# Optimization experiments

Hardware: AMD Instinct MI355X
Metric: run time of the kernel (lower is better)

Reference implementation:

```python
import jax, jax.numpy as jnp
import numpy as np

NEG_SLOPE = 0.2  # PyG GATConv default


def gat_layer(x, src, dst, W, a_src, a_dst, b, heads, ch, num_nodes):
    # x: [N, F_in]; W: [F_in, heads*ch]; a_src/a_dst: [heads, ch]; b: [heads*ch]
    h = (x @ W).reshape(num_nodes, heads, ch)                      # [N,H,C]
    al_s = jnp.einsum('nhc,hc->nh', h, a_src)                      # [N,H]
    al_d = jnp.einsum('nhc,hc->nh', h, a_dst)                      # [N,H]
    e = jax.nn.leaky_relu(al_s[src] + al_d[dst], NEG_SLOPE)        # [E,H]
    # segment softmax over incoming edges of each destination node
    emax = jax.ops.segment_max(e, dst, num_segments=num_nodes)     # [N,H]
    ee = jnp.exp(e - emax[dst])
    denom = jax.ops.segment_sum(ee, dst, num_segments=num_nodes)   # [N,H]
    alpha = ee / denom[dst]                                        # [E,H]
    msg = h[src] * alpha[..., None]                                # [E,H,C]
    out = jax.ops.segment_sum(msg, dst, num_segments=num_nodes)    # [N,H,C]
    return out.reshape(num_nodes, heads * ch) + b


def setup_inputs() -> dict:
    key = jax.random.key(0)
    ks = jax.random.split(key, 12)
    N, F_in, H1, C1, OUT = 50000, 128, 6, 32, 2
    E = 800000
    x = jax.random.normal(ks[0], (N, F_in), dtype=jnp.float32)
    edge_index = jax.random.randint(ks[1], (2, E), 0, N, dtype=jnp.int64)
    s = 0.1
    return {
        'x': x,
        'edge_index': edge_index,
        'W1': jax.random.normal(ks[2], (F_in, H1 * C1), dtype=jnp.float32) * s,
        'a1_src': jax.random.normal(ks[3], (H1, C1), dtype=jnp.float32) * s,
        'a1_dst': jax.random.normal(ks[4], (H1, C1), dtype=jnp.float32) * s,
        'b1': jnp.zeros((H1 * C1,), dtype=jnp.float32),
        'W2': jax.random.normal(ks[5], (H1 * C1, 1 * OUT), dtype=jnp.float32) * s,
        'a2_src': jax.random.normal(ks[6], (1, OUT), dtype=jnp.float32) * s,
        'a2_dst': jax.random.normal(ks[7], (1, OUT), dtype=jnp.float32) * s,
        'b2': jnp.zeros((OUT,), dtype=jnp.float32),
    }


def reference(x, edge_index, W1, a1_src, a1_dst, b1, W2, a2_src, a2_dst, b2):
    N = x.shape[0]
    loop = jnp.arange(N, dtype=edge_index.dtype)
    src = jnp.concatenate([edge_index[0], loop])  # add_self_loops=True (PyG default)
    dst = jnp.concatenate([edge_index[1], loop])
    h = gat_layer(x, src, dst, W1, a1_src, a1_dst, b1, heads=6, ch=32, num_nodes=N)
    h = jax.nn.relu(h)
    h = gat_layer(h, src, dst, W2, a2_src, a2_dst, b2, heads=1, ch=2, num_nodes=N)
    return jax.nn.log_softmax(h, axis=1)
```

## Files before the change

kernel.cpp:

```cpp
#include <hip/hip_runtime.h>
#include <hip/hip_fp16.h>

#define LRELU(v) ((v) > 0.0f ? (v) : 0.2f * (v))

constexpr int F_IN = 128;
constexpr int NH1  = 6;
constexpr int D1   = 192;

typedef _Float16 half8 __attribute__((ext_vector_type(8)));
typedef float floatx4 __attribute__((ext_vector_type(4)));

__device__ __forceinline__ void wave_lds_fence() {
  __builtin_amdgcn_wave_barrier();
  asm volatile("s_waitcnt lgkmcnt(0)" ::: "memory");
  __builtin_amdgcn_wave_barrier();
}

__global__ __launch_bounds__(256) void k_hist(const float* __restrict__ W1,
                                              __half* __restrict__ w1t,
                                              const int* __restrict__ dst,
                                              int* __restrict__ cnt,
                                              int* __restrict__ pose, int N, int E) {
  int tid = blockIdx.x * 256 + threadIdx.x;
  if (tid < F_IN * D1) {
    int k = tid / D1, n = tid - k * D1;
    w1t[(size_t)n * F_IN + k] = __float2half(W1[tid]);
  }
  if (tid < E) {
    int s = blockIdx.x & 7;
    pose[tid] = atomicAdd(&cnt[s * N + dst[tid]], 1);
  }
}

__global__ __launch_bounds__(256) void k_gemm1(const float* __restrict__ x,
                                               const __half* __restrict__ w1t,
                                               const float* __restrict__ a1s,
                                               const float* __restrict__ a1d,
                                               __half* __restrict__ h1h,
                                               float* __restrict__ als,
                                               float* __restrict__ ald, int N) {
  int wv = blockIdx.x * 4 + (threadIdx.x >> 6);
  int m0 = wv * 16;
  if (m0 >= N) return;
  int lane = threadIdx.x & 63;
  int ln15 = lane & 15, q = lane >> 4;

  float avs[12], avd[12];
#pragma unroll
  for (int f = 0; f < 12; ++f) {
    int idx = (f >> 1) * 32 + (f & 1) * 16 + ln15;
    avs[f] = a1s[idx];
    avd[f] = a1d[idx];
  }

  floatx4 acc[12];
#pragma unroll
  for (int f = 0; f < 12; ++f) acc[f] = (floatx4){0.f, 0.f, 0.f, 0.f};

  int arowi = m0 + ln15;
  if (arowi >= N) arowi = N - 1;
  const float* arow = x + (size_t)arowi * F_IN + q * 8;
#pragma unroll
  for (int kc = 0; kc < F_IN; kc += 32) {
    float4 u0 = *(const float4*)(arow + kc);
    float4 u1 = *(const float4*)(arow + kc + 4);
    half8 a;
    a[0] = (_Float16)u0.x; a[1] = (_Float16)u0.y; a[2] = (_Float16)u0.z; a[3] = (_Float16)u0.w;
    a[4] = (_Float16)u1.x; a[5] = (_Float16)u1.y; a[6] = (_Float16)u1.z; a[7] = (_Float16)u1.w;
#pragma unroll
    for (int f = 0; f < 12; ++f) {
      half8 b = *(const half8*)(w1t + (size_t)(16 * f + ln15) * F_IN + kc + q * 8);
      acc[f] = __builtin_amdgcn_mfma_f32_16x16x32_f16(a, b, acc[f], 0, 0, 0);
    }
  }

#pragma unroll
  for (int f = 0; f < 12; ++f) {
#pragma unroll
    for (int r = 0; r < 4; ++r) {
      int n = m0 + q * 4 + r;
      if (n < N) h1h[(size_t)n * D1 + 16 * f + ln15] = __float2half(acc[f][r]);
    }
  }

#pragma unroll
  for (int r = 0; r < 4; ++r) {
    float ps[6] = {0.f, 0.f, 0.f, 0.f, 0.f, 0.f};
    float pd[6] = {0.f, 0.f, 0.f, 0.f, 0.f, 0.f};
#pragma unroll
    for (int f = 0; f < 12; ++f) {
      ps[f >> 1] = fmaf(acc[f][r], avs[f], ps[f >> 1]);
      pd[f >> 1] = fmaf(acc[f][r], avd[f], pd[f >> 1]);
    }
#pragma unroll
    for (int h = 0; h < 6; ++h) {
#pragma unroll
      for (int m = 8; m; m >>= 1) {
        ps[h] += __shfl_xor(ps[h], m);
        pd[h] += __shfl_xor(pd[h], m);
      }
    }
    float os = 0.f, od = 0.f;
#pragma unroll
    for (int h = 0; h < 6; ++h)
      if (ln15 == h) { os = ps[h]; od = pd[h]; }
    int n = m0 + q * 4 + r;
    if (ln15 < 6 && n < N) {
      als[(size_t)n * 6 + ln15] = os;
      ald[(size_t)n * 6 + ln15] = od;
    }
  }
}

__global__ void k_scanA(const int* __restrict__ cnt, int* __restrict__ spre,
                        int* __restrict__ offs, int* __restrict__ bsum, int N) {
  int t = threadIdx.x;
  int idx = blockIdx.x * 256 + t;
  int lane = t & 63, w = t >> 6;
  int run = 0;
#pragma unroll
  for (int s = 0; s < 8; ++s) {
    int c = (idx < N) ? cnt[s * N + idx] : 0;
    if (idx < N) spre[s * N + idx] = run;
    run += c;
  }
  int v = run;
  int incl = v;
#pragma unroll
  for (int d = 1; d < 64; d <<= 1) {
    int u = __shfl_up(incl, d);
    if (lane >= d) incl += u;
  }
  __shared__ int wt[4];
  if (lane == 63) wt[w] = incl;
  __syncthreads();
  int woff = 0;
  for (int i = 0; i < w; ++i) woff += wt[i];
  if (idx < N) offs[idx] = woff + incl - v;
  if (t == 255) bsum[blockIdx.x] = woff + incl;
}

__global__ void k_scanB(int* __restrict__ bsum, int* __restrict__ boff, int NB) {
  int t = threadIdx.x;
  int lane = t & 63, w = t >> 6;
  int v = (t < NB) ? bsum[t] : 0;
  int incl = v;
#pragma unroll
  for (int d = 1; d < 64; d <<= 1) {
    int u = __shfl_up(incl, d);
    if (lane >= d) incl += u;
  }
  __shared__ int wt[4];
  if (lane == 63) wt[w] = incl;
  __syncthreads();
  int woff = 0;
  for (int i = 0; i < w; ++i) woff += wt[i];
  if (t < NB) boff[t] = woff + incl - v;
}

__global__ void k_scanC(int* __restrict__ offs, const int* __restrict__ boff,
                        const int* __restrict__ bsum, int N, int NB) {
  int idx = blockIdx.x * 256 + threadIdx.x;
  if (idx < N) offs[idx] += boff[blockIdx.x];
  if (idx == 0) offs[N] = boff[NB - 1] + bsum[NB - 1];
}

__global__ __launch_bounds__(256) void k_place(const int* __restrict__ src,
                                               const int* __restrict__ dst,
                                               const int* __restrict__ offs,
                                               const int* __restrict__ spre,
                                               const int* __restrict__ pose,
                                               int* __restrict__ ssort, int N, int E) {
  int e = blockIdx.x * 256 + threadIdx.x;
  if (e < E) {
    int d = dst[e];
    int s = (e >> 8) & 7;
    ssort[offs[d] + spre[s * N + d] + pose[e]] = src[e];
  }
}

__global__ __launch_bounds__(256) void k_agg1(
    const __half* __restrict__ h1h, const float* __restrict__ als, const float* __restrict__ ald,
    const int* __restrict__ offs, const int* __restrict__ srcs,
    const float* __restrict__ b1, const float* __restrict__ W2,
    const float* __restrict__ a2s, const float* __restrict__ a2d,
    float4* __restrict__ pk, int N) {
  __shared__ float wbuf[4][64][9];
  int wid = threadIdx.x >> 6, lane = threadIdx.x & 63;
  int d = blockIdx.x * 4 + wid;
  if (d >= N) return;
  int off = offs[d], cnt = offs[d + 1] - off;
  int tot = cnt + 1;

  float aldh[6];
  {
    const float* ap = ald + (size_t)d * 6;
    float2 q0 = *(const float2*)ap, q1 = *(const float2*)(ap + 2), q2 = *(const float2*)(ap + 4);
    aldh[0] = q0.x; aldh[1] = q0.y; aldh[2] = q1.x;
    aldh[3] = q1.y; aldh[4] = q2.x; aldh[5] = q2.y;
  }

  float dh[6] = {0.f, 0.f, 0.f, 0.f, 0.f, 0.f};
  int nchunk = (tot + 63) >> 6;

  float a0 = 0.f, a1 = 0.f, a2 = 0.f;
  const int hw = lane >> 4;
  const int hh = 4 + (lane >> 5);

  auto body = [&](int j) {
    float w_a = wbuf[wid][j][hw];
    float w_b = wbuf[wid][j][hh];
    int soff = __float_as_int(wbuf[wid][j][6]);
    const __half* hp = (const __half*)((const char*)h1h + soff);
    float2 v = __half22float2(*(const __half2*)(hp + 2 * lane));
    float vh = __half2float(hp[128 + lane]);
    a0 = fmaf(w_a, v.x, a0);
    a1 = fmaf(w_a, v.y, a1);
    a2 = fmaf(w_b, vh, a2);
  };
  auto jloop = [&](int jmax) {
    int j = 0;
    for (; j + 3 < jmax; j += 4) { body(j); body(j + 1); body(j + 2); body(j + 3); }
    for (; j < jmax; ++j) body(j);
  };

  if (nchunk == 1) {
    float wreg[6];
    int sreg = 0;
    if (lane < tot) {
      int s = (lane == cnt) ? d : srcs[off + lane];
      sreg = s;
      const float* ap = als + (size_t)s * 6;
      float2 p0 = *(const float2*)ap, p1 = *(const float2*)(ap + 2), p2 = *(const float2*)(ap + 4);
      float ev[6] = {p0.x, p0.y, p1.x, p1.y, p2.x, p2.y};
#pragma unroll
      for (int h = 0; h < 6; ++h) {
        float e = ev[h] + aldh[h];
        e = LRELU(e);
        wreg[h] = __expf(e);
        dh[h] = wreg[h];
      }
    }
#pragma unroll
    for (int h = 0; h < 6; ++h) {
#pragma unroll
      for (int m = 32; m; m >>= 1) dh[h] += __shfl_xor(dh[h], m);
      dh[h] = 1.0f / dh[h];
    }
    if (lane < tot) {
#pragma unroll
      for (int h = 0; h < 6; ++h) wbuf[wid][lane][h] = wreg[h] * dh[h];
      wbuf[wid][lane][6] = __int_as_float(sreg * (D1 * 2));
    }
    wave_lds_fence();
    jloop(tot);
  } else {
    for (int c = 0; c < nchunk; ++c) {
      int i = c * 64 + lane;
      if (i < tot) {
        int s = (i == cnt) ? d : srcs[off + i];
        const float* ap = als + (size_t)s * 6;
        float2 p0 = *(const float2*)ap, p1 = *(const float2*)(ap + 2), p2 = *(const float2*)(ap + 4);
        float ev[6] = {p0.x, p0.y, p1.x, p1.y, p2.x, p2.y};
#pragma unroll
        for (int h = 0; h < 6; ++h) {
          float e = ev[h] + aldh[h];
          e = LRELU(e);
          dh[h] += __expf(e);
        }
      }
    }
#pragma unroll
    for (int h = 0; h < 6; ++h) {
#pragma unroll
      for (int m = 32; m; m >>= 1) dh[h] += __shfl_xor(dh[h], m);
      dh[h] = 1.0f / dh[h];
    }
    for (int c = 0; c < nchunk; ++c) {
      int i = c * 64 + lane;
      if (i < tot) {
        int s = (i == cnt) ? d : srcs[off + i];
        const float* ap = als + (size_t)s * 6;
        float2 p0 = *(const float2*)ap, p1 = *(const float2*)(ap + 2), p2 = *(const float2*)(ap + 4);
        float ev[6] = {p0.x, p0.y, p1.x, p1.y, p2.x, p2.y};
#pragma unroll
        for (int h = 0; h < 6; ++h) {
          float e = ev[h] + aldh[h];
          e = LRELU(e);
          wbuf[wid][lane][h] = __expf(e) * dh[h];
        }
        wbuf[wid][lane][6] = __int_as_float(s * (D1 * 2));
      }
      wave_lds_fence();
      int jmax = tot - c * 64;
      if (jmax > 64) jmax = 64;
      jloop(jmax);
      wave_lds_fence();
    }
  }

  float2 bv = *(const float2*)(b1 + 2 * lane);
  float v0 = fmaxf(a0 + bv.x, 0.f);
  float v1 = fmaxf(a1 + bv.y, 0.f);
  float v2 = fmaxf(a2 + b1[128 + lane], 0.f);
  float4 ww = *(const float4*)(W2 + 4 * lane);
  float2 wh = *(const float2*)(W2 + (128 + lane) * 2);
  float s0 = v0 * ww.x + v1 * ww.z + v2 * wh.x;
  float s1 = v0 * ww.y + v1 * ww.w + v2 * wh.y;
#pragma unroll
  for (int m = 32; m; m >>= 1) {
    s0 += __shfl_xor(s0, m);
    s1 += __shfl_xor(s1, m);
  }
  if (lane == 0) {
    pk[d] = make_float4(s0, s1,
                        s0 * a2s[0] + s1 * a2s[1],
                        s0 * a2d[0] + s1 * a2d[1]);
  }
}

__global__ __launch_bounds__(256) void k_agg2(
    const float4* __restrict__ pk, const int* __restrict__ offs,
    const int* __restrict__ srcs, const float* __restrict__ b2,
    float* __restrict__ out, int N) {
  int tid = blockIdx.x * 256 + threadIdx.x;
  int g = tid >> 3, r = tid & 7;
  if (g >= N) return;
  int off = offs[g], cnt = offs[g + 1] - off;
  int tot = cnt + 1;
  float ad = pk[g].w;
  float den = 0.f, o0 = 0.f, o1 = 0.f;
  for (int i = r; i < tot; i += 8) {
    int s = (i == cnt) ? g : srcs[off + i];
    float4 p = pk[s];
    float e = p.z + ad;
    e = LRELU(e);
    float a = __expf(e);
    den += a;
    o0 = fmaf(a, p.x, o0);
    o1 = fmaf(a, p.y, o1);
  }
#pragma unroll
  for (int m = 4; m; m >>= 1) {
    den += __shfl_xor(den, m);
    o0 += __shfl_xor(o0, m);
    o1 += __shfl_xor(o1, m);
  }
  if (r == 0) {
    float inv = 1.0f / den;
    o0 = o0 * inv + b2[0];
    o1 = o1 * inv + b2[1];
    float mm = fmaxf(o0, o1);
    float l = mm + logf(__expf(o0 - mm) + __expf(o1 - mm));
    *(float2*)(out + (size_t)g * 2) = make_float2(o0 - l, o1 - l);
  }
}

extern "C" void kernel_launch(void* const* d_in, const int* in_sizes, int n_in,
                              void* d_out, int out_size, void* d_ws, size_t ws_size,
                              hipStream_t stream) {
  const float* x   = (const float*)d_in[0];
  const int*   ei  = (const int*)d_in[1];
  const float* W1  = (const float*)d_in[2];
  const float* a1s = (const float*)d_in[3];
  const float* a1d = (const float*)d_in[4];
  const float* b1  = (const float*)d_in[5];
  const float* W2  = (const float*)d_in[6];
  const float* a2s = (const float*)d_in[7];
  const float* a2d = (const float*)d_in[8];
  const float* b2  = (const float*)d_in[9];
  float* out = (float*)d_out;

  const int N = in_sizes[0] / F_IN;
  const int E = in_sizes[1] / 2;
  const int* srcp = ei;
  const int* dstp = ei + E;

  char* w = (char*)d_ws;
  auto alloc = [&](size_t bytes) {
    char* p = w;
    w += (bytes + 255) & ~(size_t)255;
    return p;
  };
  __half* h1h   = (__half*)alloc((size_t)N * D1 * 2);
  __half* w1t   = (__half*)alloc((size_t)F_IN * D1 * 2);
  float* als    = (float*)alloc((size_t)N * NH1 * 4);
  float* ald    = (float*)alloc((size_t)N * NH1 * 4);
  float4* pk    = (float4*)alloc((size_t)N * 16);
  int*   cnt    = (int*)alloc((size_t)N * 8 * 4);
  int*   spre   = (int*)alloc((size_t)N * 8 * 4);
  int*   offs   = (int*)alloc((size_t)(N + 1) * 4);
  int*   pose   = (int*)alloc((size_t)E * 4);
  int*   bsum   = (int*)alloc(1024);
  int*   boff   = (int*)alloc(1024);
  int*   ssort  = (int*)alloc((size_t)E * 4);

  const int NB = (N + 255) / 256;

  hipMemsetAsync(cnt, 0, (size_t)N * 8 * 4, stream);

  k_hist<<<(E + 255) / 256, 256, 0, stream>>>(W1, w1t, dstp, cnt, pose, N, E);

  int nwave = (N + 15) / 16;
  k_gemm1<<<(nwave + 3) / 4, 256, 0, stream>>>(x, w1t, a1s, a1d, h1h, als, ald, N);

  k_scanA<<<NB, 256, 0, stream>>>(cnt, spre, offs, bsum, N);
  k_scanB<<<1, 256, 0, stream>>>(bsum, boff, NB);
  k_scanC<<<NB, 256, 0, stream>>>(offs, boff, bsum, N, NB);
  k_place<<<(E + 255) / 256, 256, 0, stream>>>(srcp, dstp, offs, spre, pose, ssort, N, E);

  k_agg1<<<(N + 3) / 4, 256, 0, stream>>>(h1h, als, ald, offs, ssort, b1, W2,
                                          a2s, a2d, pk, N);
  k_agg2<<<(N * 8 + 255) / 256, 256, 0, stream>>>(pk, offs, ssort, b2, out, N);
}
```

Baseline: 237.7 us.

## Fuse histogram with GEMM, stage W1 in LDS, single-block scan

Result: slower. 291.2 us (+22.5%).

```diff
diff --git a/kernel.cpp b/kernel.cpp
--- a/kernel.cpp
+++ b/kernel.cpp
@@ -16,32 +16,21 @@
   __builtin_amdgcn_wave_barrier();
 }
 
-__global__ __launch_bounds__(256) void k_hist(const float* __restrict__ W1,
-                                              __half* __restrict__ w1t,
-                                              const int* __restrict__ dst,
-                                              int* __restrict__ cnt,
-                                              int* __restrict__ pose, int N, int E) {
-  int tid = blockIdx.x * 256 + threadIdx.x;
-  if (tid < F_IN * D1) {
-    int k = tid / D1, n = tid - k * D1;
-    w1t[(size_t)n * F_IN + k] = __float2half(W1[tid]);
-  }
-  if (tid < E) {
-    int s = blockIdx.x & 7;
-    pose[tid] = atomicAdd(&cnt[s * N + dst[tid]], 1);
-  }
-}
-
-__global__ __launch_bounds__(256) void k_gemm1(const float* __restrict__ x,
-                                               const __half* __restrict__ w1t,
-                                               const float* __restrict__ a1s,
-                                               const float* __restrict__ a1d,
-                                               __half* __restrict__ h1h,
-                                               float* __restrict__ als,
-                                               float* __restrict__ ald, int N) {
-  int wv = blockIdx.x * 4 + (threadIdx.x >> 6);
+__global__ __launch_bounds__(256) void k_fused(
+    const int* __restrict__ dst, int* __restrict__ cnt, int* __restrict__ pose,
+    const float* __restrict__ x, const float* __restrict__ W1,
+    const float* __restrict__ a1s, const float* __restrict__ a1d,
+    __half* __restrict__ h1h, float* __restrict__ als, float* __restrict__ ald,
+    int N, int E, int HB) {
+  if ((int)blockIdx.x < HB) {
+    int e = blockIdx.x * 256 + threadIdx.x;
+    if (e < E) pose[e] = atomicAdd(&cnt[dst[e]], 1);
+    return;
+  }
+
+  __shared__ _Float16 wlds[192][40];
+  int wv = ((int)blockIdx.x - HB) * 4 + (threadIdx.x >> 6);
   int m0 = wv * 16;
-  if (m0 >= N) return;
   int lane = threadIdx.x & 63;
   int ln15 = lane & 15, q = lane >> 4;
 
@@ -60,8 +49,16 @@
   int arowi = m0 + ln15;
   if (arowi >= N) arowi = N - 1;
   const float* arow = x + (size_t)arowi * F_IN + q * 8;
+
 #pragma unroll
   for (int kc = 0; kc < F_IN; kc += 32) {
+    __syncthreads();
+    for (int j = threadIdx.x; j < 192 * 32; j += 256) {
+      int kk = j / 192, n = j - kk * 192;
+      wlds[n][kk] = (_Float16)W1[(size_t)(kc + kk) * D1 + n];
+    }
+    __syncthreads();
+
     float4 u0 = *(const float4*)(arow + kc);
     float4 u1 = *(const float4*)(arow + kc + 4);
     half8 a;
@@ -69,7 +66,7 @@
     a[4] = (_Float16)u1.x; a[5] = (_Float16)u1.y; a[6] = (_Float16)u1.z; a[7] = (_Float16)u1.w;
 #pragma unroll
     for (int f = 0; f < 12; ++f) {
-      half8 b = *(const half8*)(w1t + (size_t)(16 * f + ln15) * F_IN + kc + q * 8);
+      half8 b = *(const half8*)(&wlds[16 * f + ln15][q * 8]);
       acc[f] = __builtin_amdgcn_mfma_f32_16x16x32_f16(a, b, acc[f], 0, 0, 0);
     }
   }
@@ -112,70 +109,58 @@
   }
 }
 
-__global__ void k_scanA(const int* __restrict__ cnt, int* __restrict__ spre,
-                        int* __restrict__ offs, int* __restrict__ bsum, int N) {
-  int t = threadIdx.x;
-  int idx = blockIdx.x * 256 + t;
-  int lane = t & 63, w = t >> 6;
-  int run = 0;
-#pragma unroll
-  for (int s = 0; s < 8; ++s) {
-    int c = (idx < N) ? cnt[s * N + idx] : 0;
-    if (idx < N) spre[s * N + idx] = run;
-    run += c;
-  }
-  int v = run;
-  int incl = v;
-#pragma unroll
-  for (int d = 1; d < 64; d <<= 1) {
-    int u = __shfl_up(incl, d);
-    if (lane >= d) incl += u;
-  }
-  __shared__ int wt[4];
-  if (lane == 63) wt[w] = incl;
-  __syncthreads();
-  int woff = 0;
-  for (int i = 0; i < w; ++i) woff += wt[i];
-  if (idx < N) offs[idx] = woff + incl - v;
-  if (t == 255) bsum[blockIdx.x] = woff + incl;
-}
-
-__global__ void k_scanB(int* __restrict__ bsum, int* __restrict__ boff, int NB) {
-  int t = threadIdx.x;
-  int lane = t & 63, w = t >> 6;
-  int v = (t < NB) ? bsum[t] : 0;
-  int incl = v;
-#pragma unroll
-  for (int d = 1; d < 64; d <<= 1) {
-    int u = __shfl_up(incl, d);
-    if (lane >= d) incl += u;
-  }
-  __shared__ int wt[4];
-  if (lane == 63) wt[w] = incl;
-  __syncthreads();
-  int woff = 0;
-  for (int i = 0; i < w; ++i) woff += wt[i];
-  if (t < NB) boff[t] = woff + incl - v;
-}
-
-__global__ void k_scanC(int* __restrict__ offs, const int* __restrict__ boff,
-                        const int* __restrict__ bsum, int N, int NB) {
-  int idx = blockIdx.x * 256 + threadIdx.x;
-  if (idx < N) offs[idx] += boff[blockIdx.x];
-  if (idx == 0) offs[N] = boff[NB - 1] + bsum[NB - 1];
+__global__ __launch_bounds__(1024) void k_scan(const int* __restrict__ cnt,
+                                               int* __restrict__ offs, int N) {
+  constexpr int MAXR = 52;
+  int t = threadIdx.x, lane = t & 63, wid = t >> 6;
+  int R = (N + 1023) >> 10;
+  __shared__ int wsum[16];
+  int v[MAXR];
+#pragma unroll
+  for (int r = 0; r < MAXR; ++r) {
+    int i = (r << 10) + t;
+    v[r] = (r < R && i < N) ? cnt[i] : 0;
+  }
+  int carry = 0;
+#pragma unroll
+  for (int r = 0; r < MAXR; ++r) {
+    if (r >= R) break;
+    int incl = v[r];
+#pragma unroll
+    for (int d = 1; d < 64; d <<= 1) {
+      int u = __shfl_up(incl, d);
+      if (lane >= d) incl += u;
+    }
+    if (lane == 63) wsum[wid] = incl;
+    __syncthreads();
+    if (t < 16) {
+      int s = wsum[t];
+#pragma unroll
+      for (int d = 1; d < 16; d <<= 1) {
+        int u = __shfl_up(s, d);
+        if (t >= d) s += u;
+      }
+      wsum[t] = s;
+    }
+    __syncthreads();
+    int wexcl = wid ? wsum[wid - 1] : 0;
+    int total = wsum[15];
+    int i = (r << 10) + t;
+    if (i < N) offs[i] = carry + wexcl + incl - v[r];
+    carry += total;
+    __syncthreads();
+  }
+  if (t == 0) offs[N] = carry;
 }
 
 __global__ __launch_bounds__(256) void k_place(const int* __restrict__ src,
                                                const int* __restrict__ dst,
                                                const int* __restrict__ offs,
-                                               const int* __restrict__ spre,
                                                const int* __restrict__ pose,
-                                               int* __restrict__ ssort, int N, int E) {
+                                               int* __restrict__ ssort, int E) {
   int e = blockIdx.x * 256 + threadIdx.x;
   if (e < E) {
-    int d = dst[e];
-    int s = (e >> 8) & 7;
-    ssort[offs[d] + spre[s * N + d] + pose[e]] = src[e];
+    ssort[offs[dst[e]] + pose[e]] = src[e];
   }
 }
 
@@ -382,33 +367,24 @@
     w += (bytes + 255) & ~(size_t)255;
     return p;
   };
-  __half* h1h   = (__half*)alloc((size_t)N * D1 * 2);
-  __half* w1t   = (__half*)alloc((size_t)F_IN * D1 * 2);
+  __half* h1h   = (__half*)alloc((size_t)N * D1 * 2 + 256);
   float* als    = (float*)alloc((size_t)N * NH1 * 4);
   float* ald    = (float*)alloc((size_t)N * NH1 * 4);
   float4* pk    = (float4*)alloc((size_t)N * 16);
-  int*   cnt    = (int*)alloc((size_t)N * 8 * 4);
-  int*   spre   = (int*)alloc((size_t)N * 8 * 4);
+  int*   cnt    = (int*)alloc((size_t)N * 4);
   int*   offs   = (int*)alloc((size_t)(N + 1) * 4);
   int*   pose   = (int*)alloc((size_t)E * 4);
-  int*   bsum   = (int*)alloc(1024);
-  int*   boff   = (int*)alloc(1024);
   int*   ssort  = (int*)alloc((size_t)E * 4);
 
-  const int NB = (N + 255) / 256;
-
-  hipMemsetAsync(cnt, 0, (size_t)N * 8 * 4, stream);
-
-  k_hist<<<(E + 255) / 256, 256, 0, stream>>>(W1, w1t, dstp, cnt, pose, N, E);
-
-  int nwave = (N + 15) / 16;
-  k_gemm1<<<(nwave + 3) / 4, 256, 0, stream>>>(x, w1t, a1s, a1d, h1h, als, ald, N);
-
-  k_scanA<<<NB, 256, 0, stream>>>(cnt, spre, offs, bsum, N);
-  k_scanB<<<1, 256, 0, stream>>>(bsum, boff, NB);
-  k_scanC<<<NB, 256, 0, stream>>>(offs, boff, bsum, N, NB);
-  k_place<<<(E + 255) / 256, 256, 0, stream>>>(srcp, dstp, offs, spre, pose, ssort, N, E);
-
+  const int HB = (E + 255) / 256;
+  const int GB = ((N + 15) / 16 + 3) / 4;
+
+  hipMemsetAsync(cnt, 0, (size_t)N * 4, stream);
+
+  k_fused<<<HB + GB, 256, 0, stream>>>(dstp, cnt, pose, x, W1, a1s, a1d,
+                                       h1h, als, ald, N, E, HB);
+  k_scan<<<1, 1024, 0, stream>>>(cnt, offs, N);
+  k_place<<<(E + 255) / 256, 256, 0, stream>>>(srcp, dstp, offs, pose, ssort, E);
   k_agg1<<<(N + 3) / 4, 256, 0, stream>>>(h1h, als, ald, offs, ssort, b1, W2,
                                           a2s, a2d, pk, N);
   k_agg2<<<(N * 8 + 255) / 256, 256, 0, stream>>>(pk, offs, ssort, b2, out, N);
```
